# Kernel tuning notes

Measured on AMD Instinct MI355X. Metric: run time of the kernel, lower is better.

Reference implementation:

```python
import jax, jax.numpy as jnp
import numpy as np

N_STATE = 128      # HiPPO state size (hardcoded N=128 in module)
SEQ = 8192         # sequence length
D_HEAD = 16        # d_model=128 // n_head=8, used only for score scaling
OUT_DIM = 1000     # hardcoded self.out_dim
STEP = 1e-3        # step_size


def _legs_matrices(N):
    # HiPPO-LegS: A[n,k] = -sqrt(2n+1)sqrt(2k+1) (n>k), -(n+1) (n==k), 0 else; B[n]=sqrt(2n+1)
    n = np.arange(N, dtype=np.float64)
    pre = np.sqrt(2.0 * n + 1.0)
    A = -np.tril(pre[:, None] * pre[None, :], -1) - np.diag(n + 1.0)
    B = pre.copy()
    return A, B


def setup_inputs() -> dict:
    key = jax.random.key(0)
    kq, kk, kv, kw = jax.random.split(key, 4)
    A_np, B_np = _legs_matrices(N_STATE)
    A = jnp.asarray(A_np, jnp.float32)
    B = jnp.asarray(B_np, jnp.float32)
    # ZOH discretization (GBT_alpha=2.0 > 1 in repo => zero-order hold)
    GA = jax.scipy.linalg.expm(STEP * A)                       # (N, N)
    GB = jnp.linalg.solve(A, (GA - jnp.eye(N_STATE)) @ B)      # (N,)
    # xavier-uniform proj kernel (128 -> 1000), zero bias
    lim = float(np.sqrt(6.0 / (N_STATE + OUT_DIM)))
    Wp = jax.random.uniform(kw, (N_STATE, OUT_DIM), jnp.float32, -lim, lim)
    bp = jnp.zeros((OUT_DIM,), jnp.float32)
    return {
        "query": jax.random.normal(kq, (SEQ, 1), jnp.float32),
        "key": jax.random.normal(kk, (SEQ, 1), jnp.float32),
        "value": jax.random.normal(kv, (SEQ, 1), jnp.float32),
        "GA": GA,
        "GB": GB,
        "Wp": Wp,
        "bp": bp,
    }


def _hippo_scan(GA, GB, fs):
    # fs: (3, S) scalar input sequences; carry c: (3, N)
    def step(c, ft):
        c = c @ GA.T + ft[:, None] * GB[None, :]
        return c, c
    c0 = jnp.zeros((fs.shape[0], GA.shape[0]), GA.dtype)
    _, cs = jax.lax.scan(step, c0, fs.T)   # cs: (S, 3, N)
    return cs


def reference(query, key, value, GA, GB, Wp, bp):
    fs = jnp.stack([query[:, 0], key[:, 0], value[:, 0]])  # (3, S)
    cs = _hippo_scan(GA, GB, fs)                            # (S, 3, N)
    q, k, v = cs[:, 0, :], cs[:, 1, :], cs[:, 2, :]         # (S, N) each
    score = (q @ k.T) / jnp.sqrt(jnp.asarray(D_HEAD, q.dtype))  # (S, S)
    attn = jax.nn.softmax(score, axis=-1)
    context = attn @ v                                      # (S, N)
    out = context @ Wp + bp                                 # (S, OUT_DIM)
    return out, attn
```

## Files before the change

### kernel.cpp

```cpp
#include <hip/hip_runtime.h>

static constexpr int N  = 128;
static constexpr int S  = 8192;
static constexpr int L  = 128;
static constexpr int NC = 64;
static constexpr int OD = 1000;
static constexpr int KSPLIT = 16;
#define SCL 0.25f


__global__ void k_copyT(const float* __restrict__ GA, float* __restrict__ QT1){
  int idx = blockIdx.x*256 + threadIdx.x;
  int m = idx >> 7, n = idx & 127;
  QT1[idx] = GA[n*N + m];
}

__global__ __launch_bounds__(256) void k_powmm(float* QT, int mlev){
  int i = blockIdx.z + 1;
  const float* Am = QT + (size_t)mlev*(N*N);
  const float* Ai = QT + (size_t)i*(N*N);
  float* C = QT + (size_t)(mlev+i)*(N*N);
  __shared__ __align__(16) float As[16][68];
  __shared__ __align__(16) float Bs[16][68];
  int bm = blockIdx.y, bn = blockIdx.x;
  int tx = threadIdx.x, ty = threadIdx.y;
  int tid = ty*16 + tx;
  float acc[4][4] = {};
  for (int kt = 0; kt < N; kt += 16){
    int row = tid >> 2, kc = (tid & 3) << 2;
    float4 av = *(const float4*)(Am + (size_t)(bm*64+row)*N + kt + kc);
    As[kc+0][row]=av.x; As[kc+1][row]=av.y; As[kc+2][row]=av.z; As[kc+3][row]=av.w;
    int bk = tid >> 4, c0 = (tid & 15) << 2;
    *(float4*)&Bs[bk][c0] = *(const float4*)(Ai + (size_t)(kt+bk)*N + bn*64 + c0);
    __syncthreads();
#pragma unroll
    for (int kk = 0; kk < 16; ++kk){
      float4 a = *(const float4*)&As[kk][ty*4];
      float4 b = *(const float4*)&Bs[kk][tx*4];
      float aa[4]={a.x,a.y,a.z,a.w}, bb[4]={b.x,b.y,b.z,b.w};
#pragma unroll
      for (int ii=0; ii<4; ++ii)
#pragma unroll
        for (int jj=0; jj<4; ++jj) acc[ii][jj] += aa[ii]*bb[jj];
    }
    __syncthreads();
  }
#pragma unroll
  for (int ii=0; ii<4; ++ii){
    float4 vst = make_float4(acc[ii][0],acc[ii][1],acc[ii][2],acc[ii][3]);
    *(float4*)(C + (size_t)(bm*64+ty*4+ii)*N + bn*64 + tx*4) = vst;
  }
}

__global__ void k_g(const float* __restrict__ QT, const float* __restrict__ GB,
                    float* __restrict__ g){
  int kb = blockIdx.x;
  int n = threadIdx.x;
  if (kb == 0){ g[n] = GB[n]; return; }
  const float* Qk = QT + (size_t)kb*(N*N);
  float acc = 0.0f;
  for (int m = 0; m < N; ++m) acc += Qk[m*N + n]*GB[m];
  g[kb*N + n] = acc;
}

__global__ __launch_bounds__(256) void k_fill_local(const float* __restrict__ fq,
                             const float* __restrict__ fk, const float* __restrict__ fv,
                             const float* __restrict__ g, float* __restrict__ cs){
  int tile = blockIdx.x;
  int s = blockIdx.y, j = blockIdx.z;
  const float* f = (s==0)? fq : (s==1)? fk : fv;
  __shared__ float flp[256];
  __shared__ __align__(16) float Bs[16][68];
  int tx = threadIdx.x, ty = threadIdx.y;
  int tid = ty*16 + tx;
  flp[tid] = (tid < 128) ? 0.0f : f[j*L + tid - 128];
  int ti = tile >> 1, tj = tile & 1;
  float acc[4][4] = {};
  int kmax = (ti == 0) ? 64 : 128;
  for (int kt = 0; kt < kmax; kt += 16){
    int bk = tid >> 4, c0 = (tid & 15) << 2;
    *(float4*)&Bs[bk][c0] = *(const float4*)(g + (size_t)(kt+bk)*N + tj*64 + c0);
    __syncthreads();
#pragma unroll
    for (int kk = 0; kk < 16; ++kk){
      float4 b = *(const float4*)&Bs[kk][tx*4];
      int base = 128 + ti*64 + ty*4 - kt - kk;
      float aa[4] = {flp[base], flp[base+1], flp[base+2], flp[base+3]};
      float bb[4] = {b.x, b.y, b.z, b.w};
#pragma unroll
      for (int ii=0; ii<4; ++ii)
#pragma unroll
        for (int jj=0; jj<4; ++jj) acc[ii][jj] += aa[ii]*bb[jj];
    }
    __syncthreads();
  }
#pragma unroll
  for (int ii=0; ii<4; ++ii){
    int row = ti*64 + ty*4 + ii;
    float4 vst = make_float4(acc[ii][0],acc[ii][1],acc[ii][2],acc[ii][3]);
    *(float4*)(cs + ((size_t)s*S + (size_t)j*L + row)*N + tj*64 + tx*4) = vst;
  }
}

__global__ void k_bscan(const float* __restrict__ QT, const float* __restrict__ cs,
                        float* __restrict__ bounds){
  __shared__ float bc[3][N];
  __shared__ float bnx[3][N];
  int tid = threadIdx.x;
  int s = tid >> 7, n = tid & 127;
  const float* QL = QT + (size_t)L*(N*N);
  bc[s][n] = 0.0f;
  bounds[(0*3+s)*N + n] = 0.0f;
  __syncthreads();
  for (int j = 0; j < NC; ++j){
    float acc = cs[((size_t)s*S + (size_t)j*L + 127)*N + n];
    for (int m = 0; m < N; ++m) acc += QL[m*N+n]*bc[s][m];
    bnx[s][n] = acc;
    bounds[((j+1)*3+s)*N + n] = acc;
    __syncthreads();
    bc[s][n] = bnx[s][n];
    __syncthreads();
  }
}

__global__ __launch_bounds__(256) void k_fill_bound(const float* __restrict__ QT,
                          const float* __restrict__ bounds, float* __restrict__ cs){
  int i = blockIdx.x;
  int jg = blockIdx.y;
  __shared__ float Qs[N*N];
  int tid = threadIdx.x;
  int p = tid >> 7, n = tid & 127;
  const float* Qg = QT + (size_t)(i+1)*(N*N);
  for (int idx = tid; idx < N*N; idx += 256) Qs[idx] = Qg[idx];
  __syncthreads();
  for (int r = 0; r < 24; ++r){
    int task = jg*48 + p*24 + r;
    int j = task/3, s = task - 3*j;
    const float* b = bounds + (size_t)task*N;
    float a0=0.f, a1=0.f, a2=0.f, a3=0.f;
    for (int m = 0; m < N; m += 4){
      a0 += Qs[(m+0)*N+n]*b[m+0];
      a1 += Qs[(m+1)*N+n]*b[m+1];
      a2 += Qs[(m+2)*N+n]*b[m+2];
      a3 += Qs[(m+3)*N+n]*b[m+3];
    }
    cs[((size_t)s*S + (size_t)j*L + i)*N + n] += (a0+a1)+(a2+a3);
  }
}

__global__ __launch_bounds__(256) void k_score(const float* __restrict__ cs,
                                               float* __restrict__ attn){
  const float* A = cs;
  const float* B = cs + (size_t)S*N;
  __shared__ __align__(16) float As[16][132];
  __shared__ __align__(16) float Bs[16][132];
  int bm = blockIdx.y, bn = blockIdx.x;
  int tx = threadIdx.x, ty = threadIdx.y;
  int tid = ty*16 + tx;
  float acc[8][8] = {};
  for (int kt = 0; kt < N; kt += 16){
#pragma unroll
    for (int ld = 0; ld < 2; ++ld){
      int idx = tid + ld*256;
      int r2 = idx >> 2, k2 = (idx & 3) << 2;
      float4 av = *(const float4*)(A + (size_t)(bm*128+r2)*N + kt + k2);
      As[k2+0][r2]=av.x; As[k2+1][r2]=av.y; As[k2+2][r2]=av.z; As[k2+3][r2]=av.w;
      float4 bv = *(const float4*)(B + (size_t)(bn*128+r2)*N + kt + k2);
      Bs[k2+0][r2]=bv.x; Bs[k2+1][r2]=bv.y; Bs[k2+2][r2]=bv.z; Bs[k2+3][r2]=bv.w;
    }
    __syncthreads();
#pragma unroll
    for (int kk = 0; kk < 16; ++kk){
      float4 a0 = *(const float4*)&As[kk][ty*8];
      float4 a1 = *(const float4*)&As[kk][ty*8+4];
      float4 b0 = *(const float4*)&Bs[kk][tx*4];
      float4 b1 = *(const float4*)&Bs[kk][64+tx*4];
      float aa[8]={a0.x,a0.y,a0.z,a0.w,a1.x,a1.y,a1.z,a1.w};
      float bb[8]={b0.x,b0.y,b0.z,b0.w,b1.x,b1.y,b1.z,b1.w};
#pragma unroll
      for (int ii=0; ii<8; ++ii)
#pragma unroll
        for (int jj=0; jj<8; ++jj) acc[ii][jj] += aa[ii]*bb[jj];
    }
    __syncthreads();
  }
#pragma unroll
  for (int ii=0; ii<8; ++ii){
    size_t r = (size_t)(bm*128 + ty*8 + ii)*S + (size_t)bn*128;
    float4 v0 = make_float4(acc[ii][0]*SCL, acc[ii][1]*SCL, acc[ii][2]*SCL, acc[ii][3]*SCL);
    float4 v1 = make_float4(acc[ii][4]*SCL, acc[ii][5]*SCL, acc[ii][6]*SCL, acc[ii][7]*SCL);
    *(float4*)(attn + r + tx*4)      = v0;
    *(float4*)(attn + r + 64 + tx*4) = v1;
  }
}

__global__ __launch_bounds__(256) void k_softmax(float* __restrict__ attn){
  __shared__ __align__(16) float rowb[S];
  __shared__ float red[256];
  int t = blockIdx.x;
  int tid = threadIdx.x;
  float4* g4 = (float4*)(attn + (size_t)t*S);
  float4* r4 = (float4*)rowb;
  float mx = -3.0e38f;
  for (int u = tid; u < S/4; u += 256){
    float4 v = g4[u];
    r4[u] = v;
    mx = fmaxf(mx, fmaxf(fmaxf(v.x,v.y), fmaxf(v.z,v.w)));
  }
  red[tid] = mx; __syncthreads();
  for (int st = 128; st > 0; st >>= 1){
    if (tid < st) red[tid] = fmaxf(red[tid], red[tid+st]);
    __syncthreads();
  }
  mx = red[0];
  __syncthreads();
  float sum = 0.0f;
  for (int u = tid; u < S/4; u += 256){
    float4 v = r4[u];
    v.x = __expf(v.x - mx); v.y = __expf(v.y - mx);
    v.z = __expf(v.z - mx); v.w = __expf(v.w - mx);
    r4[u] = v;
    sum += v.x + v.y + v.z + v.w;
  }
  red[tid] = sum; __syncthreads();
  for (int st = 128; st > 0; st >>= 1){
    if (tid < st) red[tid] += red[tid+st];
    __syncthreads();
  }
  float inv = 1.0f / red[0];
  for (int u = tid; u < S/4; u += 256){
    float4 v = r4[u];
    v.x *= inv; v.y *= inv; v.z *= inv; v.w *= inv;
    g4[u] = v;
  }
}

__global__ __launch_bounds__(256) void k_context(const float* __restrict__ attn,
                       const float* __restrict__ vs, float* __restrict__ dst, int mode){
  __shared__ __align__(16) float As[16][132];
  __shared__ __align__(16) float Bs[16][132];
  int kz = blockIdx.x;
  int bm = blockIdx.y;
  int tx = threadIdx.x, ty = threadIdx.y;
  int tid = ty*16 + tx;
  const int KC = S / KSPLIT;
  int k0 = kz*KC;
  float acc[8][8] = {};
  for (int kt = 0; kt < KC; kt += 16){
#pragma unroll
    for (int ld = 0; ld < 2; ++ld){
      int idx = tid + ld*256;
      int r2 = idx >> 2, k2 = (idx & 3) << 2;
      float4 av = *(const float4*)(attn + (size_t)(bm*128+r2)*S + k0 + kt + k2);
      As[k2+0][r2]=av.x; As[k2+1][r2]=av.y; As[k2+2][r2]=av.z; As[k2+3][r2]=av.w;
      int bk = idx >> 5, c0 = (idx & 31) << 2;
      *(float4*)&Bs[bk][c0] = *(const float4*)(vs + (size_t)(k0+kt+bk)*N + c0);
    }
    __syncthreads();
#pragma unroll
    for (int kk = 0; kk < 16; ++kk){
      float4 a0 = *(const float4*)&As[kk][ty*8];
      float4 a1 = *(const float4*)&As[kk][ty*8+4];
      float4 b0 = *(const float4*)&Bs[kk][tx*4];
      float4 b1 = *(const float4*)&Bs[kk][64+tx*4];
      float aa[8]={a0.x,a0.y,a0.z,a0.w,a1.x,a1.y,a1.z,a1.w};
      float bb[8]={b0.x,b0.y,b0.z,b0.w,b1.x,b1.y,b1.z,b1.w};
#pragma unroll
      for (int ii=0; ii<8; ++ii)
#pragma unroll
        for (int jj=0; jj<8; ++jj) acc[ii][jj] += aa[ii]*bb[jj];
    }
    __syncthreads();
  }
  if (mode == 0){
    float* P = dst + (size_t)kz*S*N;
#pragma unroll
    for (int ii=0; ii<8; ++ii){
      int r = bm*128 + ty*8 + ii;
      float4 v0 = make_float4(acc[ii][0],acc[ii][1],acc[ii][2],acc[ii][3]);
      float4 v1 = make_float4(acc[ii][4],acc[ii][5],acc[ii][6],acc[ii][7]);
      *(float4*)(P + (size_t)r*N + tx*4)      = v0;
      *(float4*)(P + (size_t)r*N + 64 + tx*4) = v1;
    }
  } else {
#pragma unroll
    for (int ii=0; ii<8; ++ii){
      int r = bm*128 + ty*8 + ii;
#pragma unroll
      for (int jj=0; jj<4; ++jj){
        atomicAdd(&dst[(size_t)r*N + tx*4 + jj],      acc[ii][jj]);
        atomicAdd(&dst[(size_t)r*N + 64 + tx*4 + jj], acc[ii][4+jj]);
      }
    }
  }
}

__global__ __launch_bounds__(256) void k_reduce(const float* __restrict__ part,
                                                float* __restrict__ ctx){
  size_t idx = (size_t)blockIdx.x*256 + threadIdx.x;
  const float4* p4 = (const float4*)part;
  float4 acc = p4[idx];
  const size_t stride = (size_t)S*N/4;
#pragma unroll
  for (int kz = 1; kz < KSPLIT; ++kz){
    float4 v = p4[(size_t)kz*stride + idx];
    acc.x += v.x; acc.y += v.y; acc.z += v.z; acc.w += v.w;
  }
  ((float4*)ctx)[idx] = acc;
}

__global__ __launch_bounds__(256) void k_out(const float* __restrict__ ctx,
                   const float* __restrict__ Wp, const float* __restrict__ bp,
                   float* __restrict__ out){
  __shared__ __align__(16) float As[16][68];
  __shared__ __align__(16) float Bs[16][68];
  int bn = blockIdx.x;
  int bm = blockIdx.y;
  int tx = threadIdx.x, ty = threadIdx.y;
  int tid = ty*16 + tx;
  float acc[4][4] = {};
  for (int kt = 0; kt < N; kt += 16){
    int row = tid >> 2, kc = (tid & 3) << 2;
    float4 av = *(const float4*)(ctx + (size_t)(bm*64+row)*N + kt + kc);
    As[kc+0][row]=av.x; As[kc+1][row]=av.y; As[kc+2][row]=av.z; As[kc+3][row]=av.w;
    int bk = tid >> 4, c0 = (tid & 15) << 2;
#pragma unroll
    for (int jj = 0; jj < 4; ++jj){
      int c = bn*64 + c0 + jj;
      Bs[bk][c0+jj] = (c < OD) ? Wp[(size_t)(kt+bk)*OD + c] : 0.0f;
    }
    __syncthreads();
#pragma unroll
    for (int kk = 0; kk < 16; ++kk){
      float4 a = *(const float4*)&As[kk][ty*4];
      float4 b = *(const float4*)&Bs[kk][tx*4];
      float aa[4]={a.x,a.y,a.z,a.w}, bb[4]={b.x,b.y,b.z,b.w};
#pragma unroll
      for (int ii=0; ii<4; ++ii)
#pragma unroll
        for (int jj=0; jj<4; ++jj) acc[ii][jj] += aa[ii]*bb[jj];
    }
    __syncthreads();
  }
#pragma unroll
  for (int ii=0; ii<4; ++ii){
    int r = bm*64 + ty*4 + ii;
#pragma unroll
    for (int jj=0; jj<4; ++jj){
      int c = bn*64 + tx*4 + jj;
      if (c < OD) out[(size_t)r*OD + c] = acc[ii][jj] + bp[c];
    }
  }
}

extern "C" void kernel_launch(void* const* d_in, const int* in_sizes, int n_in,
                              void* d_out, int out_size, void* d_ws, size_t ws_size,
                              hipStream_t stream){
  const float* fq = (const float*)d_in[0];
  const float* fk = (const float*)d_in[1];
  const float* fv = (const float*)d_in[2];
  const float* GA = (const float*)d_in[3];
  const float* GB = (const float*)d_in[4];
  const float* Wp = (const float*)d_in[5];
  const float* bp = (const float*)d_in[6];
  float* out  = (float*)d_out;
  float* attn = out + (size_t)S*OD;

  float* ws     = (float*)d_ws;
  float* QT     = ws;
  float* g      = QT + (size_t)129*N*N;
  float* bounds = g + (size_t)L*N;
  float* cs     = bounds + (size_t)(NC+1)*3*N;
  float* ctx    = cs + (size_t)3*S*N;
  float* part   = ctx + (size_t)S*N;
  size_t need_part = ((size_t)(part - ws) + (size_t)KSPLIT*S*N) * sizeof(float);
  bool use_part = (ws_size >= need_part);

  k_copyT<<<64, 256, 0, stream>>>(GA, QT + (size_t)N*N);
  for (int m = 1; m < L; m <<= 1)
    k_powmm<<<dim3(2,2,m), dim3(16,16), 0, stream>>>(QT, m);
  k_g<<<128, 128, 0, stream>>>(QT, GB, g);
  k_fill_local<<<dim3(4,3,NC), dim3(16,16), 0, stream>>>(fq, fk, fv, g, cs);
  k_bscan<<<1, 384, 0, stream>>>(QT, cs, bounds);
  k_fill_bound<<<dim3(L,4), 256, 0, stream>>>(QT, bounds, cs);
  k_score<<<dim3(S/128, S/128), dim3(16,16), 0, stream>>>(cs, attn);
  k_softmax<<<S, 256, 0, stream>>>(attn);
  if (use_part){
    k_context<<<dim3(KSPLIT, S/128), dim3(16,16), 0, stream>>>(attn, cs + (size_t)2*S*N, part, 0);
    k_reduce<<<(S*N/4)/256, 256, 0, stream>>>(part, ctx);
  } else {
    hipMemsetAsync(ctx, 0, (size_t)S*N*sizeof(float), stream);
    k_context<<<dim3(KSPLIT, S/128), dim3(16,16), 0, stream>>>(attn, cs + (size_t)2*S*N, ctx, 1);
  }
  k_out<<<dim3(16, S/64), dim3(16,16), 0, stream>>>(ctx, Wp, bp, out);
}
```

Measured before the change: 1.038 ms.

## Use split-bf16 MFMA for score and context GEMMs

```diff
diff --git a/kernel.cpp b/kernel.cpp
--- a/kernel.cpp
+++ b/kernel.cpp
@@ -7,6 +7,21 @@
 static constexpr int OD = 1000;
 static constexpr int KSPLIT = 16;
 #define SCL 0.25f
+
+typedef unsigned short u16;
+typedef __attribute__((ext_vector_type(4))) unsigned short us4;
+typedef __attribute__((ext_vector_type(8))) unsigned short us8;
+typedef __attribute__((ext_vector_type(8))) short bf16x8;
+typedef __attribute__((ext_vector_type(4))) float f32x4;
+
+__device__ __forceinline__ u16 f2bf(float x){
+  unsigned u = __float_as_uint(x);
+  u += 0x7FFFu + ((u >> 16) & 1u);
+  return (u16)(u >> 16);
+}
+__device__ __forceinline__ float bf2f(u16 h){
+  return __uint_as_float(((unsigned)h) << 16);
+}
 
 
 __global__ void k_copyT(const float* __restrict__ GA, float* __restrict__ QT1){
@@ -148,50 +163,97 @@
   }
 }
 
-__global__ __launch_bounds__(256) void k_score(const float* __restrict__ cs,
-                                               float* __restrict__ attn){
-  const float* A = cs;
-  const float* B = cs + (size_t)S*N;
-  __shared__ __align__(16) float As[16][132];
-  __shared__ __align__(16) float Bs[16][132];
+__global__ void k_split_qk(const float* __restrict__ cs,
+                           u16* __restrict__ sh, u16* __restrict__ sl){
+  size_t i = ((size_t)blockIdx.x*256 + threadIdx.x) << 2;
+  float4 v = *(const float4*)(cs + i);
+  us4 h, l;
+  h[0]=f2bf(v.x); l[0]=f2bf(v.x - bf2f(h[0]));
+  h[1]=f2bf(v.y); l[1]=f2bf(v.y - bf2f(h[1]));
+  h[2]=f2bf(v.z); l[2]=f2bf(v.z - bf2f(h[2]));
+  h[3]=f2bf(v.w); l[3]=f2bf(v.w - bf2f(h[3]));
+  *(us4*)(sh + i) = h;
+  *(us4*)(sl + i) = l;
+}
+
+__global__ __launch_bounds__(256) void k_split_vT(const float* __restrict__ vs,
+                           u16* __restrict__ vth, u16* __restrict__ vtl){
+  __shared__ u16 Th[128*72];
+  __shared__ u16 Tl[128*72];
+  int t0 = blockIdx.x * 64;
+  int tid = threadIdx.x;
+  for (int c = tid; c < 2048; c += 256){
+    int i = c >> 5, n0 = (c & 31) << 2;
+    float4 v = *(const float4*)(vs + (size_t)(t0 + i)*N + n0);
+    u16 h;
+    h = f2bf(v.x); Th[(n0+0)*72 + i] = h; Tl[(n0+0)*72 + i] = f2bf(v.x - bf2f(h));
+    h = f2bf(v.y); Th[(n0+1)*72 + i] = h; Tl[(n0+1)*72 + i] = f2bf(v.y - bf2f(h));
+    h = f2bf(v.z); Th[(n0+2)*72 + i] = h; Tl[(n0+2)*72 + i] = f2bf(v.z - bf2f(h));
+    h = f2bf(v.w); Th[(n0+3)*72 + i] = h; Tl[(n0+3)*72 + i] = f2bf(v.w - bf2f(h));
+  }
+  __syncthreads();
+  for (int c = tid; c < 1024; c += 256){
+    int n = c >> 3, tc = (c & 7) << 3;
+    *(us8*)(vth + (size_t)n*S + t0 + tc) = *(const us8*)&Th[n*72 + tc];
+    *(us8*)(vtl + (size_t)n*S + t0 + tc) = *(const us8*)&Tl[n*72 + tc];
+  }
+}
+
+__global__ __launch_bounds__(256) void k_score_mfma(
+    const u16* __restrict__ qh, const u16* __restrict__ ql,
+    const u16* __restrict__ kh, const u16* __restrict__ kl,
+    float* __restrict__ attn){
+  __shared__ u16 Ah[128*40], Al[128*40], Bh[128*40], Bl[128*40];
   int bm = blockIdx.y, bn = blockIdx.x;
-  int tx = threadIdx.x, ty = threadIdx.y;
-  int tid = ty*16 + tx;
-  float acc[8][8] = {};
-  for (int kt = 0; kt < N; kt += 16){
-#pragma unroll
-    for (int ld = 0; ld < 2; ++ld){
-      int idx = tid + ld*256;
-      int r2 = idx >> 2, k2 = (idx & 3) << 2;
-      float4 av = *(const float4*)(A + (size_t)(bm*128+r2)*N + kt + k2);
-      As[k2+0][r2]=av.x; As[k2+1][r2]=av.y; As[k2+2][r2]=av.z; As[k2+3][r2]=av.w;
-      float4 bv = *(const float4*)(B + (size_t)(bn*128+r2)*N + kt + k2);
-      Bs[k2+0][r2]=bv.x; Bs[k2+1][r2]=bv.y; Bs[k2+2][r2]=bv.z; Bs[k2+3][r2]=bv.w;
-    }
-    __syncthreads();
-#pragma unroll
-    for (int kk = 0; kk < 16; ++kk){
-      float4 a0 = *(const float4*)&As[kk][ty*8];
-      float4 a1 = *(const float4*)&As[kk][ty*8+4];
-      float4 b0 = *(const float4*)&Bs[kk][tx*4];
-      float4 b1 = *(const float4*)&Bs[kk][64+tx*4];
-      float aa[8]={a0.x,a0.y,a0.z,a0.w,a1.x,a1.y,a1.z,a1.w};
-      float bb[8]={b0.x,b0.y,b0.z,b0.w,b1.x,b1.y,b1.z,b1.w};
-#pragma unroll
-      for (int ii=0; ii<8; ++ii)
-#pragma unroll
-        for (int jj=0; jj<8; ++jj) acc[ii][jj] += aa[ii]*bb[jj];
-    }
-    __syncthreads();
-  }
-#pragma unroll
-  for (int ii=0; ii<8; ++ii){
-    size_t r = (size_t)(bm*128 + ty*8 + ii)*S + (size_t)bn*128;
-    float4 v0 = make_float4(acc[ii][0]*SCL, acc[ii][1]*SCL, acc[ii][2]*SCL, acc[ii][3]*SCL);
-    float4 v1 = make_float4(acc[ii][4]*SCL, acc[ii][5]*SCL, acc[ii][6]*SCL, acc[ii][7]*SCL);
-    *(float4*)(attn + r + tx*4)      = v0;
-    *(float4*)(attn + r + 64 + tx*4) = v1;
-  }
+  int tid = threadIdx.x;
+  int lane = tid & 63, w = tid >> 6;
+  int wr = w >> 1, wc = w & 1;
+  f32x4 acc[4][4] = {};
+  int rA = wr*64 + (lane & 15);
+  int rB = wc*64 + (lane & 15);
+  int kg = (lane >> 4) << 3;
+  for (int kt = 0; kt < N; kt += 32){
+    for (int c = tid; c < 512; c += 256){
+      int r = c >> 2, k8 = (c & 3) << 3;
+      size_t ga = (size_t)(bm*128 + r)*N + kt + k8;
+      size_t gb = (size_t)(bn*128 + r)*N + kt + k8;
+      int lo = r*40 + k8;
+      *(us8*)&Ah[lo] = *(const us8*)(qh + ga);
+      *(us8*)&Al[lo] = *(const us8*)(ql + ga);
+      *(us8*)&Bh[lo] = *(const us8*)(kh + gb);
+      *(us8*)&Bl[lo] = *(const us8*)(kl + gb);
+    }
+    __syncthreads();
+    bf16x8 ah[4], al[4], bh[4], bl[4];
+#pragma unroll
+    for (int mi = 0; mi < 4; ++mi){
+      ah[mi] = *(const bf16x8*)&Ah[(rA + mi*16)*40 + kg];
+      al[mi] = *(const bf16x8*)&Al[(rA + mi*16)*40 + kg];
+    }
+#pragma unroll
+    for (int ni = 0; ni < 4; ++ni){
+      bh[ni] = *(const bf16x8*)&Bh[(rB + ni*16)*40 + kg];
+      bl[ni] = *(const bf16x8*)&Bl[(rB + ni*16)*40 + kg];
+    }
+#pragma unroll
+    for (int mi = 0; mi < 4; ++mi)
+#pragma unroll
+      for (int ni = 0; ni < 4; ++ni){
+        acc[mi][ni] = __builtin_amdgcn_mfma_f32_16x16x32_bf16(ah[mi], bh[ni], acc[mi][ni], 0,0,0);
+        acc[mi][ni] = __builtin_amdgcn_mfma_f32_16x16x32_bf16(ah[mi], bl[ni], acc[mi][ni], 0,0,0);
+        acc[mi][ni] = __builtin_amdgcn_mfma_f32_16x16x32_bf16(al[mi], bh[ni], acc[mi][ni], 0,0,0);
+      }
+    __syncthreads();
+  }
+  int r0 = bm*128 + wr*64 + ((lane >> 4) << 2);
+  int c0 = bn*128 + wc*64 + (lane & 15);
+#pragma unroll
+  for (int mi = 0; mi < 4; ++mi)
+#pragma unroll
+    for (int ni = 0; ni < 4; ++ni)
+#pragma unroll
+      for (int r = 0; r < 4; ++r)
+        attn[(size_t)(r0 + mi*16 + r)*S + c0 + ni*16] = acc[mi][ni][r] * SCL;
 }
 
 __global__ __launch_bounds__(256) void k_softmax(float* __restrict__ attn){
@@ -235,63 +297,81 @@
   }
 }
 
-__global__ __launch_bounds__(256) void k_context(const float* __restrict__ attn,
-                       const float* __restrict__ vs, float* __restrict__ dst, int mode){
-  __shared__ __align__(16) float As[16][132];
-  __shared__ __align__(16) float Bs[16][132];
-  int kz = blockIdx.x;
-  int bm = blockIdx.y;
-  int tx = threadIdx.x, ty = threadIdx.y;
-  int tid = ty*16 + tx;
+__global__ __launch_bounds__(256) void k_context_mfma(const float* __restrict__ attn,
+                       const u16* __restrict__ vth, const u16* __restrict__ vtl,
+                       float* __restrict__ dst, int mode){
+  __shared__ u16 Ah[128*40], Al[128*40], Bh[128*40], Bl[128*40];
+  int kz = blockIdx.x, bm = blockIdx.y;
+  int tid = threadIdx.x;
+  int lane = tid & 63, w = tid >> 6;
+  int wr = w >> 1, wc = w & 1;
   const int KC = S / KSPLIT;
   int k0 = kz*KC;
-  float acc[8][8] = {};
-  for (int kt = 0; kt < KC; kt += 16){
-#pragma unroll
-    for (int ld = 0; ld < 2; ++ld){
-      int idx = tid + ld*256;
-      int r2 = idx >> 2, k2 = (idx & 3) << 2;
-      float4 av = *(const float4*)(attn + (size_t)(bm*128+r2)*S + k0 + kt + k2);
-      As[k2+0][r2]=av.x; As[k2+1][r2]=av.y; As[k2+2][r2]=av.z; As[k2+3][r2]=av.w;
-      int bk = idx >> 5, c0 = (idx & 31) << 2;
-      *(float4*)&Bs[bk][c0] = *(const float4*)(vs + (size_t)(k0+kt+bk)*N + c0);
-    }
-    __syncthreads();
-#pragma unroll
-    for (int kk = 0; kk < 16; ++kk){
-      float4 a0 = *(const float4*)&As[kk][ty*8];
-      float4 a1 = *(const float4*)&As[kk][ty*8+4];
-      float4 b0 = *(const float4*)&Bs[kk][tx*4];
-      float4 b1 = *(const float4*)&Bs[kk][64+tx*4];
-      float aa[8]={a0.x,a0.y,a0.z,a0.w,a1.x,a1.y,a1.z,a1.w};
-      float bb[8]={b0.x,b0.y,b0.z,b0.w,b1.x,b1.y,b1.z,b1.w};
-#pragma unroll
-      for (int ii=0; ii<8; ++ii)
-#pragma unroll
-        for (int jj=0; jj<8; ++jj) acc[ii][jj] += aa[ii]*bb[jj];
-    }
-    __syncthreads();
-  }
+  f32x4 acc[4][4] = {};
+  int rA = wr*64 + (lane & 15);
+  int rB = wc*64 + (lane & 15);
+  int kg = (lane >> 4) << 3;
+  for (int kt = 0; kt < KC; kt += 32){
+    for (int c = tid; c < 1024; c += 256){
+      int r = c >> 3, c4 = (c & 7) << 2;
+      float4 v = *(const float4*)(attn + (size_t)(bm*128 + r)*S + k0 + kt + c4);
+      us4 h, l;
+      h[0]=f2bf(v.x); l[0]=f2bf(v.x - bf2f(h[0]));
+      h[1]=f2bf(v.y); l[1]=f2bf(v.y - bf2f(h[1]));
+      h[2]=f2bf(v.z); l[2]=f2bf(v.z - bf2f(h[2]));
+      h[3]=f2bf(v.w); l[3]=f2bf(v.w - bf2f(h[3]));
+      int lo = r*40 + c4;
+      *(us4*)&Ah[lo] = h;
+      *(us4*)&Al[lo] = l;
+    }
+    for (int c = tid; c < 512; c += 256){
+      int n = c >> 2, k8 = (c & 3) << 3;
+      size_t gb = (size_t)n*S + k0 + kt + k8;
+      int lo = n*40 + k8;
+      *(us8*)&Bh[lo] = *(const us8*)(vth + gb);
+      *(us8*)&Bl[lo] = *(const us8*)(vtl + gb);
+    }
+    __syncthreads();
+    bf16x8 ah[4], al[4], bh[4], bl[4];
+#pragma unroll
+    for (int mi = 0; mi < 4; ++mi){
+      ah[mi] = *(const bf16x8*)&Ah[(rA + mi*16)*40 + kg];
+      al[mi] = *(const bf16x8*)&Al[(rA + mi*16)*40 + kg];
+    }
+#pragma unroll
+    for (int ni = 0; ni < 4; ++ni){
+      bh[ni] = *(const bf16x8*)&Bh[(rB + ni*16)*40 + kg];
+      bl[ni] = *(const bf16x8*)&Bl[(rB + ni*16)*40 + kg];
+    }
+#pragma unroll
+    for (int mi = 0; mi < 4; ++mi)
+#pragma unroll
+      for (int ni = 0; ni < 4; ++ni){
+        acc[mi][ni] = __builtin_amdgcn_mfma_f32_16x16x32_bf16(ah[mi], bh[ni], acc[mi][ni], 0,0,0);
+        acc[mi][ni] = __builtin_amdgcn_mfma_f32_16x16x32_bf16(ah[mi], bl[ni], acc[mi][ni], 0,0,0);
+        acc[mi][ni] = __builtin_amdgcn_mfma_f32_16x16x32_bf16(al[mi], bh[ni], acc[mi][ni], 0,0,0);
+      }
+    __syncthreads();
+  }
+  int r0 = bm*128 + wr*64 + ((lane >> 4) << 2);
+  int c0 = wc*64 + (lane & 15);
   if (mode == 0){
     float* P = dst + (size_t)kz*S*N;
 #pragma unroll
-    for (int ii=0; ii<8; ++ii){
-      int r = bm*128 + ty*8 + ii;
-      float4 v0 = make_float4(acc[ii][0],acc[ii][1],acc[ii][2],acc[ii][3]);
-      float4 v1 = make_float4(acc[ii][4],acc[ii][5],acc[ii][6],acc[ii][7]);
-      *(float4*)(P + (size_t)r*N + tx*4)      = v0;
-      *(float4*)(P + (size_t)r*N + 64 + tx*4) = v1;
-    }
+    for (int mi = 0; mi < 4; ++mi)
+#pragma unroll
+      for (int ni = 0; ni < 4; ++ni)
+#pragma unroll
+        for (int r = 0; r < 4; ++r)
+          P[(size_t)(r0 + mi*16 + r)*N + c0 + ni*16] = acc[mi][ni][r];
   } else {
 #pragma unroll
-    for (int ii=0; ii<8; ++ii){
-      int r = bm*128 + ty*8 + ii;
-#pragma unroll
-      for (int jj=0; jj<4; ++jj){
-        atomicAdd(&dst[(size_t)r*N + tx*4 + jj],      acc[ii][jj]);
-        atomicAdd(&dst[(size_t)r*N + 64 + tx*4 + jj], acc[ii][4+jj]);
-      }
-    }
+    for (int mi = 0; mi < 4; ++mi)
+#pragma unroll
+      for (int ni = 0; ni < 4; ++ni)
+#pragma unroll
+        for (int r = 0; r < 4; ++r)
+          atomicAdd(&dst[(size_t)(r0 + mi*16 + r)*N + c0 + ni*16], acc[mi][ni][r]);
   }
 }
 
@@ -372,7 +452,11 @@
   float* bounds = g + (size_t)L*N;
   float* cs     = bounds + (size_t)(NC+1)*3*N;
   float* ctx    = cs + (size_t)3*S*N;
-  float* part   = ctx + (size_t)S*N;
+  u16*   qkh    = (u16*)(ctx + (size_t)S*N);
+  u16*   qkl    = qkh + (size_t)2*S*N;
+  u16*   vth    = qkl + (size_t)2*S*N;
+  u16*   vtl    = vth + (size_t)S*N;
+  float* part   = (float*)(vtl + (size_t)S*N);
   size_t need_part = ((size_t)(part - ws) + (size_t)KSPLIT*S*N) * sizeof(float);
   bool use_part = (ws_size >= need_part);
 
@@ -383,14 +467,19 @@
   k_fill_local<<<dim3(4,3,NC), dim3(16,16), 0, stream>>>(fq, fk, fv, g, cs);
   k_bscan<<<1, 384, 0, stream>>>(QT, cs, bounds);
   k_fill_bound<<<dim3(L,4), 256, 0, stream>>>(QT, bounds, cs);
-  k_score<<<dim3(S/128, S/128), dim3(16,16), 0, stream>>>(cs, attn);
+
+  k_split_qk<<<(2*S*N)/1024, 256, 0, stream>>>(cs, qkh, qkl);
+  k_split_vT<<<S/64, 256, 0, stream>>>(cs + (size_t)2*S*N, vth, vtl);
+
+  k_score_mfma<<<dim3(S/128, S/128), 256, 0, stream>>>(
+      qkh, qkl, qkh + (size_t)S*N, qkl + (size_t)S*N, attn);
   k_softmax<<<S, 256, 0, stream>>>(attn);
   if (use_part){
-    k_context<<<dim3(KSPLIT, S/128), dim3(16,16), 0, stream>>>(attn, cs + (size_t)2*S*N, part, 0);
+    k_context_mfma<<<dim3(KSPLIT, S/128), 256, 0, stream>>>(attn, vth, vtl, part, 0);
     k_reduce<<<(S*N/4)/256, 256, 0, stream>>>(part, ctx);
   } else {
     hipMemsetAsync(ctx, 0, (size_t)S*N*sizeof(float), stream);
-    k_context<<<dim3(KSPLIT, S/128), dim3(16,16), 0, stream>>>(attn, cs + (size_t)2*S*N, ctx, 1);
+    k_context_mfma<<<dim3(KSPLIT, S/128), 256, 0, stream>>>(attn, vth, vtl, ctx, 1);
   }
   k_out<<<dim3(16, S/64), dim3(16,16), 0, stream>>>(ctx, Wp, bp, out);
 }
```

Measured after the change: 863.2 us. -16.9%, faster.
